# Performance work log

Measured on AMD Instinct MI355X. Metric: run time of the kernel, lower is better.

## Reference

```python
import jax, jax.numpy as jnp
import numpy as np

B, N, H, I = 64, 1000, 128, 64  # batch, nodes, hidden_dim, loc-embed intermediate
BN_EPS = 1e-5
NEG_SLOPE = 0.2


def setup_inputs() -> dict:
    key = jax.random.key(0)
    ks = jax.random.split(key, 24)
    s = lambda k, shape, sc=0.05: (jax.random.normal(k, shape) * sc).astype(jnp.float32)
    d = {}
    d["locs"] = jax.random.uniform(ks[0], (B, N, 2), dtype=jnp.float32)
    # LocationEmbedding params (num_layers=1 hidden block)
    d["le_W0"] = s(ks[1], (2, I));   d["le_b0"] = jnp.zeros((I,), jnp.float32)
    d["le_W1"] = s(ks[2], (I, I));   d["le_b1"] = jnp.zeros((I,), jnp.float32)
    d["le_bn_g"] = 1.0 + s(ks[3], (I,), 0.1)
    d["le_bn_b"] = s(ks[4], (I,), 0.1)
    d["le_bn_m"] = s(ks[5], (I,), 0.1)
    d["le_bn_v"] = 0.5 + jax.random.uniform(ks[6], (I,), dtype=jnp.float32)
    d["le_Wo"] = s(ks[7], (I, H));   d["le_bo"] = jnp.zeros((H,), jnp.float32)
    # 3 GATConv layers (heads=1): lin weight (no bias), att_src, att_dst, output bias
    d["gat_W"] = s(ks[8], (3, H, H))
    d["gat_asrc"] = s(ks[9], (3, H))
    d["gat_adst"] = s(ks[10], (3, H))
    d["gat_b"] = jnp.zeros((3, H), jnp.float32)
    # 2 BatchNorm layers between GAT layers (eval mode: running stats)
    d["bn_g"] = 1.0 + s(ks[11], (2, H), 0.1)
    d["bn_b"] = s(ks[12], (2, H), 0.1)
    d["bn_m"] = s(ks[13], (2, H), 0.1)
    d["bn_v"] = 0.5 + jax.random.uniform(ks[14], (2, H), dtype=jnp.float32)
    return d


def _bn(x, g, b, m, v):
    return (x - m) * jax.lax.rsqrt(v + BN_EPS) * g + b


def _gat(x, W, a_src, a_dst, bias):
    # Dense fully-connected GAT (heads=1, self-loops included).
    h = jnp.einsum('bnc,cd->bnd', x, W)          # [B,N,H]
    e_src = jnp.einsum('bnd,d->bn', h, a_src)    # alpha contribution of source j
    e_dst = jnp.einsum('bnd,d->bn', h, a_dst)    # alpha contribution of target i
    e = e_src[:, None, :] + e_dst[:, :, None]    # e[b,i,j] for edge j->i
    e = jnp.where(e > 0, e, NEG_SLOPE * e)       # leaky_relu(0.2)
    alpha = jax.nn.softmax(e, axis=-1)           # softmax over sources j per target i
    return jnp.einsum('bij,bjc->bic', alpha, h) + bias


def reference(locs, le_W0, le_b0, le_W1, le_b1, le_bn_g, le_bn_b, le_bn_m, le_bn_v,
              le_Wo, le_bo, gat_W, gat_asrc, gat_adst, gat_b, bn_g, bn_b, bn_m, bn_v):
    # LocationEmbedding: Linear -> ReLU -> [Linear -> BN -> ReLU -> (dropout: eval)] -> Linear
    z = jax.nn.relu(locs @ le_W0 + le_b0)
    z = jax.nn.relu(_bn(z @ le_W1 + le_b1, le_bn_g, le_bn_b, le_bn_m, le_bn_v))
    x = z @ le_Wo + le_bo                        # [B,N,H]
    # [GAT -> BN -> ReLU -> (dropout: eval)] x2 -> GAT
    for l in range(2):
        x = _gat(x, gat_W[l], gat_asrc[l], gat_adst[l], gat_b[l])
        x = jax.nn.relu(_bn(x, bn_g[l], bn_b[l], bn_m[l], bn_v[l]))
    x = _gat(x, gat_W[2], gat_asrc[2], gat_adst[2], gat_b[2])
    return x                                     # [B,N,H]
```

## Files before the change

### kernel.cpp

```cpp
#include <hip/hip_runtime.h>
#include <hip/hip_bf16.h>

#define BN_EPS 1e-5f
#define NB 64
#define NN 1000
#define NP 1024
#define HD 128
#define CS 8
#define NC 125
#define XS 136

typedef short bf16x8 __attribute__((ext_vector_type(8)));
typedef float f32x4 __attribute__((ext_vector_type(4)));

__device__ __forceinline__ unsigned short f2b(float f) {
  __hip_bfloat16 h = __float2bfloat16(f);
  return *reinterpret_cast<unsigned short*>(&h);
}
__device__ __forceinline__ float b2f(unsigned short u) {
  unsigned v = ((unsigned)u) << 16;
  return __uint_as_float(v);
}
__device__ __forceinline__ unsigned tkey(float f) {
  unsigned u = __float_as_uint(f);
  return u ^ ((unsigned)((int)u >> 31) | 0x80000000u);
}
__device__ __forceinline__ float tdec(unsigned m) {
  unsigned u = (m & 0x80000000u) ? (m ^ 0x80000000u) : ~m;
  return __uint_as_float(u);
}

__global__ __launch_bounds__(256) void k_wprep(const float* __restrict__ W,
                                               unsigned short* __restrict__ WT) {
  int idx = blockIdx.x * 256 + threadIdx.x;
  int lay = idx >> 14, rem = idx & 16383;
  int n = rem >> 7, k = rem & 127;
  WT[idx] = f2b(W[lay * 16384 + k * 128 + n]);
}

__global__ __launch_bounds__(256) void k_embed_gemm(
    const float* __restrict__ locs,
    const float* __restrict__ W0, const float* __restrict__ b0,
    const float* __restrict__ W1, const float* __restrict__ b1,
    const float* __restrict__ g1, const float* __restrict__ be1,
    const float* __restrict__ m1, const float* __restrict__ v1,
    const float* __restrict__ Wo, const float* __restrict__ bo,
    const unsigned short* __restrict__ WT,
    const float* __restrict__ asrc, const float* __restrict__ adst,
    unsigned short* __restrict__ hb, float* __restrict__ es,
    float* __restrict__ ed) {
  __shared__ float z1T[64][68];
  __shared__ float z2T[64][68];
  unsigned short* xs = (unsigned short*)&z1T[0][0];
  int tid = threadIdx.x;
  long base = (long)blockIdx.x * 64;

  {
    int d = tid & 63;
    int q = tid >> 6;
    float w0x = W0[d], w0y = W0[64 + d], bb = b0[d];
#pragma unroll
    for (int g = 0; g < 4; ++g) {
      float vv[4];
#pragma unroll
      for (int i = 0; i < 4; ++i) {
        int n = g * 16 + q * 4 + i;
        float lx = locs[(base + n) * 2 + 0];
        float ly = locs[(base + n) * 2 + 1];
        vv[i] = fmaxf(fmaf(lx, w0x, fmaf(ly, w0y, bb)), 0.f);
      }
      *(float4*)&z1T[d][g * 16 + q * 4] = make_float4(vv[0], vv[1], vv[2], vv[3]);
    }
  }
  __syncthreads();

  int nt = tid & 15;
  int dt = tid >> 4;

  {
    float acc[4][4];
#pragma unroll
    for (int i = 0; i < 4; ++i)
#pragma unroll
      for (int j = 0; j < 4; ++j) acc[i][j] = 0.f;
#pragma unroll 4
    for (int k = 0; k < 64; ++k) {
      float4 zv = *(const float4*)&z1T[k][4 * nt];
      float4 wv = *(const float4*)&W1[k * 64 + 4 * dt];
      float zz[4] = {zv.x, zv.y, zv.z, zv.w};
      float ww[4] = {wv.x, wv.y, wv.z, wv.w};
#pragma unroll
      for (int i = 0; i < 4; ++i)
#pragma unroll
        for (int j = 0; j < 4; ++j) acc[i][j] = fmaf(zz[i], ww[j], acc[i][j]);
    }
    float4 b1v = *(const float4*)&b1[4 * dt];
    float4 g1v = *(const float4*)&g1[4 * dt];
    float4 bev = *(const float4*)&be1[4 * dt];
    float4 m1v = *(const float4*)&m1[4 * dt];
    float4 v1v = *(const float4*)&v1[4 * dt];
    float bbv[4] = {b1v.x, b1v.y, b1v.z, b1v.w};
    float ggv[4] = {g1v.x, g1v.y, g1v.z, g1v.w};
    float eev[4] = {bev.x, bev.y, bev.z, bev.w};
    float mmv[4] = {m1v.x, m1v.y, m1v.z, m1v.w};
    float vvv[4] = {v1v.x, v1v.y, v1v.z, v1v.w};
#pragma unroll
    for (int j = 0; j < 4; ++j) {
      float sc = ggv[j] * rsqrtf(vvv[j] + BN_EPS);
      float sh = eev[j] - mmv[j] * sc;
      float o[4];
#pragma unroll
      for (int i = 0; i < 4; ++i)
        o[i] = fmaxf(fmaf(acc[i][j] + bbv[j], sc, sh), 0.f);
      *(float4*)&z2T[4 * dt + j][4 * nt] = make_float4(o[0], o[1], o[2], o[3]);
    }
  }
  __syncthreads();

  {
    float acc[4][8];
#pragma unroll
    for (int i = 0; i < 4; ++i)
#pragma unroll
      for (int j = 0; j < 8; ++j) acc[i][j] = 0.f;
#pragma unroll 2
    for (int k = 0; k < 64; ++k) {
      float4 zv = *(const float4*)&z2T[k][4 * nt];
      float4 wa = *(const float4*)&Wo[k * 128 + 4 * dt];
      float4 wb = *(const float4*)&Wo[k * 128 + 64 + 4 * dt];
      float zz[4] = {zv.x, zv.y, zv.z, zv.w};
      float w0[4] = {wa.x, wa.y, wa.z, wa.w};
      float w1[4] = {wb.x, wb.y, wb.z, wb.w};
#pragma unroll
      for (int i = 0; i < 4; ++i) {
#pragma unroll
        for (int j = 0; j < 4; ++j) {
          acc[i][j] = fmaf(zz[i], w0[j], acc[i][j]);
          acc[i][4 + j] = fmaf(zz[i], w1[j], acc[i][4 + j]);
        }
      }
    }
    float4 bo0 = *(const float4*)&bo[4 * dt];
    float4 bo1 = *(const float4*)&bo[64 + 4 * dt];
    float bb0[4] = {bo0.x, bo0.y, bo0.z, bo0.w};
    float bb1[4] = {bo1.x, bo1.y, bo1.z, bo1.w};
#pragma unroll
    for (int i = 0; i < 4; ++i) {
      ushort4 p0, p1;
      p0.x = f2b(acc[i][0] + bb0[0]); p0.y = f2b(acc[i][1] + bb0[1]);
      p0.z = f2b(acc[i][2] + bb0[2]); p0.w = f2b(acc[i][3] + bb0[3]);
      p1.x = f2b(acc[i][4] + bb1[0]); p1.y = f2b(acc[i][5] + bb1[1]);
      p1.z = f2b(acc[i][6] + bb1[2]); p1.w = f2b(acc[i][7] + bb1[3]);
      *(ushort4*)&xs[(4 * nt + i) * XS + 4 * dt] = p0;
      *(ushort4*)&xs[(4 * nt + i) * XS + 64 + 4 * dt] = p1;
    }
  }
  __syncthreads();

  {
    int w = tid >> 6, l = tid & 63;
    long rowbase = base + w * 16;
    int r = l & 15, g = l >> 4;
    f32x4 acc[8];
#pragma unroll
    for (int n = 0; n < 8; ++n) acc[n] = {0.f, 0.f, 0.f, 0.f};
#pragma unroll
    for (int ks = 0; ks < 4; ++ks) {
      bf16x8 a = *(const bf16x8*)&xs[(w * 16 + r) * XS + ks * 32 + g * 8];
#pragma unroll
      for (int n = 0; n < 8; ++n) {
        bf16x8 bfr = *(const bf16x8*)&WT[(n * 16 + r) * 128 + ks * 32 + g * 8];
        acc[n] = __builtin_amdgcn_mfma_f32_16x16x32_bf16(a, bfr, acc[n], 0, 0, 0);
      }
    }
    float ps[4] = {0.f, 0.f, 0.f, 0.f};
    float pd[4] = {0.f, 0.f, 0.f, 0.f};
#pragma unroll
    for (int n = 0; n < 8; ++n) {
      float sa = asrc[n * 16 + r];
      float sd = adst[n * 16 + r];
#pragma unroll
      for (int rr = 0; rr < 4; ++rr) {
        float v = acc[n][rr];
        hb[(rowbase + g * 4 + rr) * 128 + n * 16 + r] = f2b(v);
        ps[rr] = fmaf(v, sa, ps[rr]);
        pd[rr] = fmaf(v, sd, pd[rr]);
      }
    }
#pragma unroll
    for (int rr = 0; rr < 4; ++rr) {
#pragma unroll
      for (int m = 1; m <= 8; m <<= 1) {
        ps[rr] += __shfl_xor(ps[rr], m, 64);
        pd[rr] += __shfl_xor(pd[rr], m, 64);
      }
    }
    if (r == 0) {
#pragma unroll
      for (int rr = 0; rr < 4; ++rr) {
        es[rowbase + g * 4 + rr] = ps[rr];
        ed[rowbase + g * 4 + rr] = pd[rr];
      }
    }
  }
}

__global__ __launch_bounds__(256) void k_gemm_e(
    const unsigned short* __restrict__ xb, const unsigned short* __restrict__ WT,
    const float* __restrict__ asrc, const float* __restrict__ adst,
    unsigned short* __restrict__ hb, float* __restrict__ es,
    float* __restrict__ ed) {
  int tid = threadIdx.x;
  int w = tid >> 6, l = tid & 63;
  long rowbase = (long)blockIdx.x * 64 + w * 16;
  int r = l & 15, g = l >> 4;

  f32x4 acc[8];
#pragma unroll
  for (int n = 0; n < 8; ++n) acc[n] = {0.f, 0.f, 0.f, 0.f};

#pragma unroll
  for (int ks = 0; ks < 4; ++ks) {
    bf16x8 a = *(const bf16x8*)&xb[(rowbase + r) * 128 + ks * 32 + g * 8];
#pragma unroll
    for (int n = 0; n < 8; ++n) {
      bf16x8 bfr = *(const bf16x8*)&WT[(n * 16 + r) * 128 + ks * 32 + g * 8];
      acc[n] = __builtin_amdgcn_mfma_f32_16x16x32_bf16(a, bfr, acc[n], 0, 0, 0);
    }
  }

  float ps[4] = {0.f, 0.f, 0.f, 0.f};
  float pd[4] = {0.f, 0.f, 0.f, 0.f};
#pragma unroll
  for (int n = 0; n < 8; ++n) {
    float sa = asrc[n * 16 + r];
    float sd = adst[n * 16 + r];
#pragma unroll
    for (int rr = 0; rr < 4; ++rr) {
      float v = acc[n][rr];
      hb[(rowbase + g * 4 + rr) * 128 + n * 16 + r] = f2b(v);
      ps[rr] = fmaf(v, sa, ps[rr]);
      pd[rr] = fmaf(v, sd, pd[rr]);
    }
  }
#pragma unroll
  for (int rr = 0; rr < 4; ++rr) {
#pragma unroll
    for (int m = 1; m <= 8; m <<= 1) {
      ps[rr] += __shfl_xor(ps[rr], m, 64);
      pd[rr] += __shfl_xor(pd[rr], m, 64);
    }
  }
  if (r == 0) {
#pragma unroll
    for (int rr = 0; rr < 4; ++rr) {
      es[rowbase + g * 4 + rr] = ps[rr];
      ed[rowbase + g * 4 + rr] = pd[rr];
    }
  }
}

#define CEX(a, b, up)                         \
  do {                                        \
    if (((a) > (b)) == (up)) {                \
      unsigned long long _t = (a);            \
      (a) = (b);                              \
      (b) = _t;                               \
    }                                         \
  } while (0)

__global__ __launch_bounds__(512) void k_scpfx(
    const float* __restrict__ es, const float* __restrict__ ed,
    const unsigned short* __restrict__ hb, float2* __restrict__ e12,
    int* __restrict__ kcut, float2* __restrict__ ab, float2* __restrict__ C12,
    unsigned short* __restrict__ hs) {
  __shared__ unsigned long long keys[NP];
  __shared__ float smem[(NC + 1) * 64];
  __shared__ float2 wtot[8];
  float2* sc = (float2*)smem;
  float (*s1)[32] = (float(*)[32])smem;
  float (*s2)[32] = (float(*)[32])(smem + (NC + 1) * 32);
  int tid = threadIdx.x, b = blockIdx.x, dq = blockIdx.y;

  for (int i = tid; i < NP; i += 512) {
    unsigned long long kk;
    if (i < NN) {
      kk = ((unsigned long long)tkey(es[b * NN + i]) << 32) | (unsigned)i;
    } else {
      kk = (0xFF800000ull << 32) | (unsigned)i;
    }
    keys[i] = kk;
  }
  __syncthreads();
  int i0 = tid * 2;
  {
    unsigned long long q0 = keys[i0], q1 = keys[i0 + 1];
    CEX(q0, q1, (i0 & 2) == 0);
    keys[i0] = q0; keys[i0 + 1] = q1;
  }
  __syncthreads();
  for (int k = 4; k <= NP; k <<= 1) {
    for (int j = k >> 1; j >= 2; j >>= 1) {
      int i = ((tid & ~(j - 1)) << 1) | (tid & (j - 1));
      int ixj = i | j;
      bool up = ((i & k) == 0);
      unsigned long long a = keys[i], c = keys[ixj];
      if ((a > c) == up) { keys[i] = c; keys[ixj] = a; }
      __syncthreads();
    }
    {
      unsigned long long q0 = keys[i0], q1 = keys[i0 + 1];
      CEX(q0, q1, (i0 & k) == 0);
      keys[i0] = q0; keys[i0 + 1] = q1;
    }
    __syncthreads();
  }

  float2 f0 = make_float2(0.f, 0.f), f1 = make_float2(0.f, 0.f);
  {
    unsigned long long k0 = keys[i0], k1 = keys[i0 + 1];
    if (i0 < NN) {
      float s = tdec((unsigned)(k0 >> 32));
      f0.x = __expf(s);
      f0.y = __expf(0.2f * s);
      if (dq == 0) e12[b * NN + i0] = f0;
    }
    if (i0 + 1 < NN) {
      float s = tdec((unsigned)(k1 >> 32));
      f1.x = __expf(s);
      f1.y = __expf(0.2f * s);
      if (dq == 0) e12[b * NN + i0 + 1] = f1;
    }
  }
  int lane = tid & 63, wid = tid >> 6;
  float tx = f0.x + f1.x, ty = f0.y + f1.y;
  float ix = tx, iy = ty;
#pragma unroll
  for (int dlt = 1; dlt < 64; dlt <<= 1) {
    float ox = __shfl_up(ix, dlt, 64);
    float oy = __shfl_up(iy, dlt, 64);
    if (lane >= dlt) { ix += ox; iy += oy; }
  }
  if (lane == 63) wtot[wid] = make_float2(ix, iy);
  __syncthreads();
  float bx = 0.f, by = 0.f;
#pragma unroll
  for (int ww = 0; ww < 8; ++ww) {
    if (ww < wid) {
      float2 t = wtot[ww];
      bx += t.x;
      by += t.y;
    }
  }
  float exx = bx + ix - tx, eyy = by + iy - ty;
  float in0x = exx + f0.x, in0y = eyy + f0.y;
  if (i0 < NN) sc[i0] = make_float2(in0x, in0y);
  if (i0 + 1 < NN) sc[i0 + 1] = make_float2(in0x + f1.x, in0y + f1.y);
  __syncthreads();

  if (dq == 0) {
    float s1tot = sc[NN - 1].x;
    for (int i = tid; i < NN; i += 512) {
      float di = ed[b * NN + i];
      unsigned tt = tkey(-di);
      int lo = 0, hi = NP;
      while (lo < hi) {
        int mid = (lo + hi) >> 1;
        if ((unsigned)(keys[mid] >> 32) <= tt) lo = mid + 1; else hi = mid;
      }
      int k = lo;
      float p1 = (k > 0) ? sc[k - 1].x : 0.f;
      float p2 = (k > 0) ? sc[k - 1].y : 0.f;
      float Ed = __expf(di);
      float Ed2 = __expf(0.2f * di);
      float den = fmaf(Ed, s1tot - p1, Ed2 * p2);
      kcut[b * NN + i] = k;
      ab[b * NN + i] = make_float2(Ed / den, Ed2 / den);
    }
  }
  __syncthreads();

  int d = tid & 31;
  int cl = tid >> 5;
  int dglob = dq * 32 + d;
  for (int c = cl; c < NC; c += 16) {
    float v1 = 0.f, v2 = 0.f;
#pragma unroll
    for (int u = 0; u < CS; ++u) {
      int j = c * CS + u;
      unsigned long long kk = keys[j];
      int p = (int)(unsigned)kk;
      float s = tdec((unsigned)(kk >> 32));
      float e1 = __expf(s), e2 = __expf(0.2f * s);
      unsigned short hraw = hb[((long)b * NN + p) * HD + dglob];
      hs[((long)b * NN + j) * HD + dglob] = hraw;
      float hv = b2f(hraw);
      v1 = fmaf(e1, hv, v1);
      v2 = fmaf(e2, hv, v2);
    }
    s1[c][d] = v1;
    s2[c][d] = v2;
  }
  __syncthreads();

  if (tid < 32) {
    float r = 0.f;
    for (int c = 0; c < NC; ++c) {
      float v = s1[c][tid];
      s1[c][tid] = r;
      r += v;
    }
    s1[NC][tid] = r;
  } else if (tid < 64) {
    int dd = tid - 32;
    float r = 0.f;
    for (int c = 0; c < NC; ++c) {
      float v = s2[c][dd];
      s2[c][dd] = r;
      r += v;
    }
    s2[NC][dd] = r;
  }
  __syncthreads();

  long basec = (long)b * (NC + 1) * HD + dq * 32;
  for (int i = tid; i < (NC + 1) * 32; i += 512) {
    int c = i >> 5, dd = i & 31;
    C12[basec + (long)c * HD + dd] = make_float2(s1[c][dd], s2[c][dd]);
  }
}

template <bool APPLY_BN>
__global__ __launch_bounds__(128) void k_out(
    const unsigned short* __restrict__ hs, const float2* __restrict__ C12,
    const float2* __restrict__ e12, const int* __restrict__ kcut,
    const float2* __restrict__ ab, const float* __restrict__ bias,
    const float* __restrict__ bng, const float* __restrict__ bnb,
    const float* __restrict__ bnm, const float* __restrict__ bnv,
    float* __restrict__ xo, unsigned short* __restrict__ xbo) {
  int d = threadIdx.x, b = blockIdx.x;
  int i0 = blockIdx.y * 8;
  float T1 = C12[((long)b * (NC + 1) + NC) * HD + d].x;
  float bs = bias[d];
  float sc = 0.f, sh = 0.f;
  if (APPLY_BN) {
    float g = bng[d], bb = bnb[d], m = bnm[d], v = bnv[d];
    sc = g * rsqrtf(v + BN_EPS);
    sh = bb - m * sc;
  }
  for (int i = i0; i < i0 + 8; ++i) {
    int k = kcut[b * NN + i];
    float2 coeff = ab[b * NN + i];
    int c = k >> 3;
    float2 base12 = C12[((long)b * (NC + 1) + c) * HD + d];
    float p1 = 0.f, p2 = 0.f;
    for (int j = c * CS; j < k; ++j) {
      float hv = b2f(hs[((long)b * NN + j) * HD + d]);
      float2 e = e12[b * NN + j];
      p1 = fmaf(e.x, hv, p1);
      p2 = fmaf(e.y, hv, p2);
    }
    float val = fmaf(coeff.x, T1 - base12.x - p1,
                     fmaf(coeff.y, base12.y + p2, bs));
    long off = ((long)b * NN + i) * HD + d;
    if (APPLY_BN) {
      xbo[off] = f2b(fmaxf(fmaf(val, sc, sh), 0.f));
    } else {
      xo[off] = val;
    }
  }
}

extern "C" void kernel_launch(void* const* d_in, const int* in_sizes, int n_in,
                              void* d_out, int out_size, void* d_ws,
                              size_t ws_size, hipStream_t stream) {
  const float* locs = (const float*)d_in[0];
  const float* le_W0 = (const float*)d_in[1];
  const float* le_b0 = (const float*)d_in[2];
  const float* le_W1 = (const float*)d_in[3];
  const float* le_b1 = (const float*)d_in[4];
  const float* le_bn_g = (const float*)d_in[5];
  const float* le_bn_b = (const float*)d_in[6];
  const float* le_bn_m = (const float*)d_in[7];
  const float* le_bn_v = (const float*)d_in[8];
  const float* le_Wo = (const float*)d_in[9];
  const float* le_bo = (const float*)d_in[10];
  const float* gat_W = (const float*)d_in[11];
  const float* gat_asrc = (const float*)d_in[12];
  const float* gat_adst = (const float*)d_in[13];
  const float* gat_b = (const float*)d_in[14];
  const float* bn_g = (const float*)d_in[15];
  const float* bn_b = (const float*)d_in[16];
  const float* bn_m = (const float*)d_in[17];
  const float* bn_v = (const float*)d_in[18];

  float* out = (float*)d_out;
  unsigned short* hb = (unsigned short*)d_ws;
  unsigned short* hs = hb + 8192000;
  unsigned short* xb = hs + 8192000;
  unsigned short* WT = xb + 8192000;
  float2* C12 = (float2*)(WT + 49152 + 64);
  float* es = (float*)(C12 + 1032192);
  float* ed = es + 64000;
  float2* e12 = (float2*)(ed + 64000);
  float2* ab = e12 + 64000;
  int* kcut = (int*)(ab + 64000);

  k_wprep<<<192, 256, 0, stream>>>(gat_W, WT);
  for (int l = 0; l < 3; ++l) {
    if (l == 0) {
      k_embed_gemm<<<1000, 256, 0, stream>>>(
          locs, le_W0, le_b0, le_W1, le_b1, le_bn_g, le_bn_b, le_bn_m,
          le_bn_v, le_Wo, le_bo, WT, gat_asrc, gat_adst, hb, es, ed);
    } else {
      k_gemm_e<<<1000, 256, 0, stream>>>(xb, WT + l * 16384,
                                         gat_asrc + l * 128,
                                         gat_adst + l * 128, hb, es, ed);
    }
    k_scpfx<<<dim3(NB, 4), 512, 0, stream>>>(es, ed, hb, e12, kcut, ab, C12,
                                             hs);
    if (l < 2) {
      k_out<true><<<dim3(NB, NC), 128, 0, stream>>>(
          hs, C12, e12, kcut, ab, gat_b + l * 128, bn_g + l * 128,
          bn_b + l * 128, bn_m + l * 128, bn_v + l * 128, nullptr, xb);
    } else {
      k_out<false><<<dim3(NB, NC), 128, 0, stream>>>(
          hs, C12, e12, kcut, ab, gat_b + 2 * 128, nullptr, nullptr, nullptr,
          nullptr, out, nullptr);
    }
  }
}
```

Measured before the change: 206.8 us.

## Fold embedding output Linear into first GAT weight and use MFMA for embed layers

Precomputes Wo·Wg0 and bo·Wg0 in the weight-prep kernel so the embedding output projection and the first GAT linear collapse into one 64→128 GEMM. The hidden 64x64 layer and the fused projection now run on bf16 MFMA instead of scalar fp32 FMA loops. The aim is to cut FLOPs and LDS traffic in the first-layer kernel. In exchange, the intermediate z activations are rounded to bf16, which adds some precision loss, and weight prep gets a small serial dot-product cost.

After: 183.7 us, median of 2. 11.2% less time.

```diff
diff --git a/kernel.cpp b/kernel.cpp
--- a/kernel.cpp
+++ b/kernel.cpp
@@ -8,7 +8,7 @@
 #define HD 128
 #define CS 8
 #define NC 125
-#define XS 136
+#define ZS 72
 
 typedef short bf16x8 __attribute__((ext_vector_type(8)));
 typedef float f32x4 __attribute__((ext_vector_type(4)));
@@ -30,28 +30,49 @@
   return __uint_as_float(u);
 }
 
-__global__ __launch_bounds__(256) void k_wprep(const float* __restrict__ W,
-                                               unsigned short* __restrict__ WT) {
+__global__ __launch_bounds__(256) void k_wprep(
+    const float* __restrict__ Wg, const float* __restrict__ W1,
+    const float* __restrict__ Wo, const float* __restrict__ bo,
+    unsigned short* __restrict__ WT, unsigned short* __restrict__ W1T,
+    unsigned short* __restrict__ WoWgT, float* __restrict__ biash) {
   int idx = blockIdx.x * 256 + threadIdx.x;
-  int lay = idx >> 14, rem = idx & 16383;
-  int n = rem >> 7, k = rem & 127;
-  WT[idx] = f2b(W[lay * 16384 + k * 128 + n]);
+  if (idx < 49152) {
+    int lay = idx >> 14, rem = idx & 16383;
+    int n = rem >> 7, k = rem & 127;
+    WT[idx] = f2b(Wg[lay * 16384 + k * 128 + n]);
+  } else if (idx < 53248) {
+    int j = idx - 49152;
+    int n = j >> 6, k = j & 63;
+    W1T[j] = f2b(W1[k * 64 + n]);
+  } else if (idx < 61440) {
+    int j = idx - 53248;
+    int c = j >> 6, i = j & 63;
+    float acc = 0.f;
+#pragma unroll 4
+    for (int d = 0; d < 128; ++d)
+      acc = fmaf(Wo[i * 128 + d], Wg[d * 128 + c], acc);
+    WoWgT[j] = f2b(acc);
+  } else if (idx < 61568) {
+    int c = idx - 61440;
+    float acc = 0.f;
+#pragma unroll 4
+    for (int d = 0; d < 128; ++d) acc = fmaf(bo[d], Wg[d * 128 + c], acc);
+    biash[c] = acc;
+  }
 }
 
 __global__ __launch_bounds__(256) void k_embed_gemm(
     const float* __restrict__ locs,
     const float* __restrict__ W0, const float* __restrict__ b0,
-    const float* __restrict__ W1, const float* __restrict__ b1,
-    const float* __restrict__ g1, const float* __restrict__ be1,
-    const float* __restrict__ m1, const float* __restrict__ v1,
-    const float* __restrict__ Wo, const float* __restrict__ bo,
-    const unsigned short* __restrict__ WT,
+    const float* __restrict__ b1, const float* __restrict__ g1,
+    const float* __restrict__ be1, const float* __restrict__ m1,
+    const float* __restrict__ v1, const unsigned short* __restrict__ W1T,
+    const unsigned short* __restrict__ WoWgT, const float* __restrict__ biash,
     const float* __restrict__ asrc, const float* __restrict__ adst,
     unsigned short* __restrict__ hb, float* __restrict__ es,
     float* __restrict__ ed) {
-  __shared__ float z1T[64][68];
-  __shared__ float z2T[64][68];
-  unsigned short* xs = (unsigned short*)&z1T[0][0];
+  __shared__ __align__(16) unsigned short z1b[64 * ZS];
+  __shared__ __align__(16) unsigned short z2b[64 * ZS];
   int tid = threadIdx.x;
   long base = (long)blockIdx.x * 64;
 
@@ -61,115 +82,59 @@
     float w0x = W0[d], w0y = W0[64 + d], bb = b0[d];
 #pragma unroll
     for (int g = 0; g < 4; ++g) {
-      float vv[4];
 #pragma unroll
       for (int i = 0; i < 4; ++i) {
         int n = g * 16 + q * 4 + i;
         float lx = locs[(base + n) * 2 + 0];
         float ly = locs[(base + n) * 2 + 1];
-        vv[i] = fmaxf(fmaf(lx, w0x, fmaf(ly, w0y, bb)), 0.f);
-      }
-      *(float4*)&z1T[d][g * 16 + q * 4] = make_float4(vv[0], vv[1], vv[2], vv[3]);
-    }
-  }
-  __syncthreads();
-
-  int nt = tid & 15;
-  int dt = tid >> 4;
+        z1b[n * ZS + d] = f2b(fmaxf(fmaf(lx, w0x, fmaf(ly, w0y, bb)), 0.f));
+      }
+    }
+  }
+  __syncthreads();
+
+  int w = tid >> 6, l = tid & 63;
+  int r = l & 15, g = l >> 4;
 
   {
-    float acc[4][4];
-#pragma unroll
-    for (int i = 0; i < 4; ++i)
-#pragma unroll
-      for (int j = 0; j < 4; ++j) acc[i][j] = 0.f;
-#pragma unroll 4
-    for (int k = 0; k < 64; ++k) {
-      float4 zv = *(const float4*)&z1T[k][4 * nt];
-      float4 wv = *(const float4*)&W1[k * 64 + 4 * dt];
-      float zz[4] = {zv.x, zv.y, zv.z, zv.w};
-      float ww[4] = {wv.x, wv.y, wv.z, wv.w};
-#pragma unroll
-      for (int i = 0; i < 4; ++i)
-#pragma unroll
-        for (int j = 0; j < 4; ++j) acc[i][j] = fmaf(zz[i], ww[j], acc[i][j]);
-    }
-    float4 b1v = *(const float4*)&b1[4 * dt];
-    float4 g1v = *(const float4*)&g1[4 * dt];
-    float4 bev = *(const float4*)&be1[4 * dt];
-    float4 m1v = *(const float4*)&m1[4 * dt];
-    float4 v1v = *(const float4*)&v1[4 * dt];
-    float bbv[4] = {b1v.x, b1v.y, b1v.z, b1v.w};
-    float ggv[4] = {g1v.x, g1v.y, g1v.z, g1v.w};
-    float eev[4] = {bev.x, bev.y, bev.z, bev.w};
-    float mmv[4] = {m1v.x, m1v.y, m1v.z, m1v.w};
-    float vvv[4] = {v1v.x, v1v.y, v1v.z, v1v.w};
-#pragma unroll
-    for (int j = 0; j < 4; ++j) {
-      float sc = ggv[j] * rsqrtf(vvv[j] + BN_EPS);
-      float sh = eev[j] - mmv[j] * sc;
-      float o[4];
-#pragma unroll
-      for (int i = 0; i < 4; ++i)
-        o[i] = fmaxf(fmaf(acc[i][j] + bbv[j], sc, sh), 0.f);
-      *(float4*)&z2T[4 * dt + j][4 * nt] = make_float4(o[0], o[1], o[2], o[3]);
+    f32x4 acc[4];
+#pragma unroll
+    for (int n = 0; n < 4; ++n) acc[n] = {0.f, 0.f, 0.f, 0.f};
+#pragma unroll
+    for (int ks = 0; ks < 2; ++ks) {
+      bf16x8 a = *(const bf16x8*)&z1b[(w * 16 + r) * ZS + ks * 32 + g * 8];
+#pragma unroll
+      for (int n = 0; n < 4; ++n) {
+        bf16x8 bfr = *(const bf16x8*)&W1T[(n * 16 + r) * 64 + ks * 32 + g * 8];
+        acc[n] = __builtin_amdgcn_mfma_f32_16x16x32_bf16(a, bfr, acc[n], 0, 0, 0);
+      }
+    }
+#pragma unroll
+    for (int n = 0; n < 4; ++n) {
+      int col = n * 16 + r;
+      float sc = g1[col] * rsqrtf(v1[col] + BN_EPS);
+      float sh = be1[col] - m1[col] * sc;
+      float bb = b1[col];
+#pragma unroll
+      for (int rr = 0; rr < 4; ++rr) {
+        float v = fmaxf(fmaf(acc[n][rr] + bb, sc, sh), 0.f);
+        z2b[(w * 16 + g * 4 + rr) * ZS + col] = f2b(v);
+      }
     }
   }
   __syncthreads();
 
   {
-    float acc[4][8];
-#pragma unroll
-    for (int i = 0; i < 4; ++i)
-#pragma unroll
-      for (int j = 0; j < 8; ++j) acc[i][j] = 0.f;
-#pragma unroll 2
-    for (int k = 0; k < 64; ++k) {
-      float4 zv = *(const float4*)&z2T[k][4 * nt];
-      float4 wa = *(const float4*)&Wo[k * 128 + 4 * dt];
-      float4 wb = *(const float4*)&Wo[k * 128 + 64 + 4 * dt];
-      float zz[4] = {zv.x, zv.y, zv.z, zv.w};
-      float w0[4] = {wa.x, wa.y, wa.z, wa.w};
-      float w1[4] = {wb.x, wb.y, wb.z, wb.w};
-#pragma unroll
-      for (int i = 0; i < 4; ++i) {
-#pragma unroll
-        for (int j = 0; j < 4; ++j) {
-          acc[i][j] = fmaf(zz[i], w0[j], acc[i][j]);
-          acc[i][4 + j] = fmaf(zz[i], w1[j], acc[i][4 + j]);
-        }
-      }
-    }
-    float4 bo0 = *(const float4*)&bo[4 * dt];
-    float4 bo1 = *(const float4*)&bo[64 + 4 * dt];
-    float bb0[4] = {bo0.x, bo0.y, bo0.z, bo0.w};
-    float bb1[4] = {bo1.x, bo1.y, bo1.z, bo1.w};
-#pragma unroll
-    for (int i = 0; i < 4; ++i) {
-      ushort4 p0, p1;
-      p0.x = f2b(acc[i][0] + bb0[0]); p0.y = f2b(acc[i][1] + bb0[1]);
-      p0.z = f2b(acc[i][2] + bb0[2]); p0.w = f2b(acc[i][3] + bb0[3]);
-      p1.x = f2b(acc[i][4] + bb1[0]); p1.y = f2b(acc[i][5] + bb1[1]);
-      p1.z = f2b(acc[i][6] + bb1[2]); p1.w = f2b(acc[i][7] + bb1[3]);
-      *(ushort4*)&xs[(4 * nt + i) * XS + 4 * dt] = p0;
-      *(ushort4*)&xs[(4 * nt + i) * XS + 64 + 4 * dt] = p1;
-    }
-  }
-  __syncthreads();
-
-  {
-    int w = tid >> 6, l = tid & 63;
     long rowbase = base + w * 16;
-    int r = l & 15, g = l >> 4;
     f32x4 acc[8];
 #pragma unroll
     for (int n = 0; n < 8; ++n) acc[n] = {0.f, 0.f, 0.f, 0.f};
 #pragma unroll
-    for (int ks = 0; ks < 4; ++ks) {
-      bf16x8 a = *(const bf16x8*)&xs[(w * 16 + r) * XS + ks * 32 + g * 8];
+    for (int ks = 0; ks < 2; ++ks) {
+      bf16x8 a = *(const bf16x8*)&z2b[(w * 16 + r) * ZS + ks * 32 + g * 8];
 #pragma unroll
       for (int n = 0; n < 8; ++n) {
-        bf16x8 bfr = *(const bf16x8*)&WT[(n * 16 + r) * 128 + ks * 32 + g * 8];
+        bf16x8 bfr = *(const bf16x8*)&WoWgT[(n * 16 + r) * 64 + ks * 32 + g * 8];
         acc[n] = __builtin_amdgcn_mfma_f32_16x16x32_bf16(a, bfr, acc[n], 0, 0, 0);
       }
     }
@@ -177,12 +142,14 @@
     float pd[4] = {0.f, 0.f, 0.f, 0.f};
 #pragma unroll
     for (int n = 0; n < 8; ++n) {
-      float sa = asrc[n * 16 + r];
-      float sd = adst[n * 16 + r];
+      int col = n * 16 + r;
+      float bh = biash[col];
+      float sa = asrc[col];
+      float sd = adst[col];
 #pragma unroll
       for (int rr = 0; rr < 4; ++rr) {
-        float v = acc[n][rr];
-        hb[(rowbase + g * 4 + rr) * 128 + n * 16 + r] = f2b(v);
+        float v = acc[n][rr] + bh;
+        hb[(rowbase + g * 4 + rr) * 128 + col] = f2b(v);
         ps[rr] = fmaf(v, sa, ps[rr]);
         pd[rr] = fmaf(v, sd, pd[rr]);
       }
@@ -499,19 +466,23 @@
   unsigned short* hs = hb + 8192000;
   unsigned short* xb = hs + 8192000;
   unsigned short* WT = xb + 8192000;
-  float2* C12 = (float2*)(WT + 49152 + 64);
+  unsigned short* W1T = WT + 49152;
+  unsigned short* WoWgT = W1T + 4096;
+  float* biash = (float*)(WoWgT + 8192 + 32);
+  float2* C12 = (float2*)(biash + 128 + 32);
   float* es = (float*)(C12 + 1032192);
   float* ed = es + 64000;
   float2* e12 = (float2*)(ed + 64000);
   float2* ab = e12 + 64000;
   int* kcut = (int*)(ab + 64000);
 
-  k_wprep<<<192, 256, 0, stream>>>(gat_W, WT);
+  k_wprep<<<241, 256, 0, stream>>>(gat_W, le_W1, le_Wo, le_bo, WT, W1T, WoWgT,
+                                   biash);
   for (int l = 0; l < 3; ++l) {
     if (l == 0) {
       k_embed_gemm<<<1000, 256, 0, stream>>>(
-          locs, le_W0, le_b0, le_W1, le_b1, le_bn_g, le_bn_b, le_bn_m,
-          le_bn_v, le_Wo, le_bo, WT, gat_asrc, gat_adst, hb, es, ed);
+          locs, le_W0, le_b0, le_b1, le_bn_g, le_bn_b, le_bn_m, le_bn_v, W1T,
+          WoWgT, biash, gat_asrc, gat_adst, hb, es, ed);
     } else {
       k_gemm_e<<<1000, 256, 0, stream>>>(xb, WT + l * 16384,
                                          gat_asrc + l * 128,
```
